# Kernel optimization log

Measured on AMD Instinct MI355X. Metric: run time of the kernel, lower is better.

The kernel has to match this reference:

```python
import jax, jax.numpy as jnp
import numpy as np

D, NH, NKV, HD, FFN = 2560, 8, 4, 256, 10240
QD = NH * HD
CTX = 4096
EPS = 1e-6


def _rms(x, eps=EPS):
    # Equivalent to F.layer_norm(cat([x,-x]), 2D): zero mean, var = mean(x^2)
    return x * jax.lax.rsqrt(jnp.mean(jnp.square(x), axis=-1, keepdims=True) + eps)


def rmsnorm(x, w):
    # Gemma-style ANERMSNorm with learnable scale (1 + w)
    return _rms(x) * (1.0 + w)


def rotate_half(x):
    x1, x2 = jnp.split(x, 2, axis=-1)
    return jnp.concatenate([-x2, x1], axis=-1)


def setup_inputs() -> dict:
    key = jax.random.key(0)
    ks = jax.random.split(key, 16)
    s = 0.02
    return {
        "x": jax.random.normal(ks[0], (1, 1, D), jnp.float32),
        "cos": jax.random.uniform(ks[1], (1, 1, HD), jnp.float32, -1.0, 1.0),
        "sin": jax.random.uniform(ks[2], (1, 1, HD), jnp.float32, -1.0, 1.0),
        "mask": jnp.zeros((1, 1, 1, CTX), jnp.float32),
        "cache_k": jax.random.normal(ks[3], (1, NKV, CTX, HD), jnp.float32),
        "cache_v": jax.random.normal(ks[4], (1, NKV, CTX, HD), jnp.float32),
        "ctx_len": CTX,
        "w_in_ln": jax.random.normal(ks[5], (D,), jnp.float32) * s,
        "w_post_attn_ln": jax.random.normal(ks[6], (D,), jnp.float32) * s,
        "w_pre_ffn_ln": jax.random.normal(ks[7], (D,), jnp.float32) * s,
        "w_post_ffn_ln": jax.random.normal(ks[8], (D,), jnp.float32) * s,
        "Wq": jax.random.normal(ks[9], (QD, D), jnp.float32) * s,
        "Wo": jax.random.normal(ks[10], (D, QD), jnp.float32) * s,
        "Wg": jax.random.normal(ks[11], (FFN, D), jnp.float32) * s,
        "Wu": jax.random.normal(ks[12], (FFN, D), jnp.float32) * s,
        "Wd": jax.random.normal(ks[13], (D, FFN), jnp.float32) * s,
    }


def reference(x, cos, sin, mask, cache_k, cache_v, ctx_len,
              w_in_ln, w_post_attn_ln, w_pre_ffn_ln, w_post_ffn_ln,
              Wq, Wo, Wg, Wu, Wd):
    rep = NH // NKV
    residual = x
    h = rmsnorm(x, w_in_ln)                      # (1,1,D)
    q = h @ Wq.T                                 # (1,1,QD)  1x1-conv == linear
    q = q.reshape(1, 1, NH, HD)
    q = _rms(q)                                  # q_norm, no learnable weight
    q = q.transpose(0, 2, 1, 3)                  # (1,NH,1,HD)
    q = q * cos[:, None] + rotate_half(q) * sin[:, None]
    k = jnp.repeat(cache_k, rep, axis=1)         # (1,NH,L,HD) GQA expand
    v = jnp.repeat(cache_v, rep, axis=1)
    scores = jnp.einsum("bhqd,bhkd->bhqk", q, k) * 1.0 + mask
    attn = jax.nn.softmax(scores, axis=-1)       # numerically stable softmax
    a = jnp.einsum("bhqk,bhkd->bhqd", attn, v)   # (1,NH,1,HD)
    a = a.transpose(0, 2, 1, 3).reshape(1, 1, QD)
    a = a @ Wo.T                                 # (1,1,D)
    x = residual + rmsnorm(a, w_post_attn_ln)
    residual = x
    h = rmsnorm(x, w_pre_ffn_ln)
    g = jax.nn.gelu(h @ Wg.T, approximate=True)  # tanh-approx GELU
    ffn = (g * (h @ Wu.T)) @ Wd.T                # GeGLU down-proj
    x = residual + rmsnorm(ffn, w_post_ffn_ln)
    return x
```

## Files before the change

kernel.cpp:

```cpp
#include <hip/hip_runtime.h>

#define D_    2560
#define NH_   8
#define NKV_  4
#define HD_   256
#define FFN_  10240
#define QD_   2048
#define CTX_  4096
#define EPSF  1e-6f
#define ACH   64

typedef float f4 __attribute__((ext_vector_type(4)));

__device__ __forceinline__ float wave_red_sum(float v) {
#pragma unroll
    for (int o = 32; o > 0; o >>= 1) v += __shfl_down(v, o, 64);
    return v;
}

__device__ __forceinline__ float wave_red_sum_b(float v) {
#pragma unroll
    for (int o = 32; o > 0; o >>= 1) v += __shfl_xor(v, o, 64);
    return v;
}

__device__ __forceinline__ float block_red_sum(float v) {
    __shared__ float s[4];
    __shared__ float tot;
    int lane = threadIdx.x & 63, w = threadIdx.x >> 6;
    v = wave_red_sum(v);
    if (lane == 0) s[w] = v;
    __syncthreads();
    if (threadIdx.x == 0) tot = s[0] + s[1] + s[2] + s[3];
    __syncthreads();
    return tot;
}

__device__ __forceinline__ float block_red_max(float v) {
    __shared__ float s[4];
    __shared__ float tot;
    int lane = threadIdx.x & 63, w = threadIdx.x >> 6;
#pragma unroll
    for (int o = 32; o > 0; o >>= 1) v = fmaxf(v, __shfl_down(v, o, 64));
    if (lane == 0) s[w] = v;
    __syncthreads();
    if (threadIdx.x == 0) tot = fmaxf(fmaxf(s[0], s[1]), fmaxf(s[2], s[3]));
    __syncthreads();
    return tot;
}

template <int CPL>
__global__ __launch_bounds__(256) void k_gemv_row(const float* __restrict__ W,
                                                  const float* __restrict__ x,
                                                  float* __restrict__ y) {
    int lane = threadIdx.x & 63;
    int row = (blockIdx.x * 256 + threadIdx.x) >> 6;
    const f4* Wr = (const f4*)W + (size_t)row * (CPL * 64) + lane;
    const f4* X = (const f4*)x + lane;
    f4 wv[CPL];
#pragma unroll
    for (int k = 0; k < CPL; k++) wv[k] = __builtin_nontemporal_load(Wr + k * 64);
    float acc = 0.f;
#pragma unroll
    for (int k = 0; k < CPL; k++) {
        f4 xx = X[k * 64];
        acc += wv[k].x * xx.x + wv[k].y * xx.y + wv[k].z * xx.z + wv[k].w * xx.w;
    }
    acc = wave_red_sum(acc);
    if (lane == 0) y[row] = acc;
}

__global__ __launch_bounds__(256) void k_geglu(const float* __restrict__ Wg,
                                               const float* __restrict__ Wu,
                                               const float* __restrict__ h,
                                               float* __restrict__ gu) {
    int lane = threadIdx.x & 63;
    int row = (blockIdx.x * 256 + threadIdx.x) >> 6;
    const f4* G = (const f4*)Wg + (size_t)row * 640 + lane;
    const f4* U = (const f4*)Wu + (size_t)row * 640 + lane;
    const f4* X = (const f4*)h + lane;
    f4 wg[10], wu[10];
#pragma unroll
    for (int k = 0; k < 10; k++) wg[k] = __builtin_nontemporal_load(G + k * 64);
#pragma unroll
    for (int k = 0; k < 10; k++) wu[k] = __builtin_nontemporal_load(U + k * 64);
    float ag = 0.f, au = 0.f;
#pragma unroll
    for (int k = 0; k < 10; k++) {
        f4 xx = X[k * 64];
        ag += wg[k].x * xx.x + wg[k].y * xx.y + wg[k].z * xx.z + wg[k].w * xx.w;
        au += wu[k].x * xx.x + wu[k].y * xx.y + wu[k].z * xx.z + wu[k].w * xx.w;
    }
#pragma unroll
    for (int o = 32; o > 0; o >>= 1) {
        ag += __shfl_down(ag, o, 64);
        au += __shfl_down(au, o, 64);
    }
    if (lane == 0) {
        float g = ag;
        float tt = tanhf(0.7978845608028654f * (g + 0.044715f * g * g * g));
        gu[row] = 0.5f * g * (1.f + tt) * au;
    }
}

__global__ __launch_bounds__(256) void k_wd(const float* __restrict__ Wd,
                                            const float* __restrict__ gu,
                                            float* __restrict__ part) {
    int lane = threadIdx.x & 63;
    int t = (blockIdx.x * 256 + threadIdx.x) >> 6;
    int half = t & 1;
    const f4* Wr = (const f4*)Wd + (size_t)t * 1280 + lane;
    const f4* X = (const f4*)gu + half * 1280 + lane;
    f4 wv[20];
#pragma unroll
    for (int k = 0; k < 20; k++) wv[k] = __builtin_nontemporal_load(Wr + k * 64);
    float acc = 0.f;
#pragma unroll
    for (int k = 0; k < 20; k++) {
        f4 xx = X[k * 64];
        acc += wv[k].x * xx.x + wv[k].y * xx.y + wv[k].z * xx.z + wv[k].w * xx.w;
    }
    acc = wave_red_sum(acc);
    if (lane == 0) part[t] = acc;
}

__global__ void k_res_rms(const float* __restrict__ res,
                          const float* __restrict__ apart, int slots,
                          const float* __restrict__ w1, float* __restrict__ out1,
                          const float* __restrict__ w2, float* __restrict__ out2) {
    const int K = D_ / 256;
    int t = threadIdx.x;
    float va[K];
    float ss = 0.f;
#pragma unroll
    for (int k = 0; k < K; k++) {
        int i = t + k * 256;
        float v = 0.f;
        for (int s = 0; s < slots; s++) v += apart[(size_t)i * slots + s];
        va[k] = v;
        ss += v * v;
    }
    float tot = block_red_sum(ss);
    float rs = rsqrtf(tot / (float)D_ + EPSF);
    float vo[K];
    float ss2 = 0.f;
#pragma unroll
    for (int k = 0; k < K; k++) {
        int i = t + k * 256;
        float r = res ? res[i] : 0.f;
        vo[k] = r + va[k] * rs * (1.f + w1[i]);
        out1[i] = vo[k];
        ss2 += vo[k] * vo[k];
    }
    if (out2) {
        float tot2 = block_red_sum(ss2);
        float rs2 = rsqrtf(tot2 / (float)D_ + EPSF);
#pragma unroll
        for (int k = 0; k < K; k++) {
            int i = t + k * 256;
            out2[i] = vo[k] * rs2 * (1.f + w2[i]);
        }
    }
}

__global__ __launch_bounds__(256) void k_attn_part(const float* __restrict__ Kc,
                                                   const float* __restrict__ V,
                                                   const float* __restrict__ qraw,
                                                   const float* __restrict__ cosv,
                                                   const float* __restrict__ sinv,
                                                   const float* __restrict__ mask,
                                                   float* __restrict__ pm,
                                                   float* __restrict__ pl,
                                                   float* __restrict__ pacc) {
    int kvh = blockIdx.x, ch = blockIdx.y;
    int lane = threadIdx.x & 63, w = threadIdx.x >> 6;
    int t = threadIdx.x;
    int h0 = 2 * kvh, h1 = h0 + 1;
    int l0 = ch * 64;
    __shared__ float s0[64], s1[64];

    const f4* q4 = (const f4*)qraw;
    f4 qr0 = q4[h0 * 64 + lane];
    f4 qr1 = q4[h1 * 64 + lane];
    float n0 = wave_red_sum_b(qr0.x * qr0.x + qr0.y * qr0.y + qr0.z * qr0.z + qr0.w * qr0.w);
    float n1 = wave_red_sum_b(qr1.x * qr1.x + qr1.y * qr1.y + qr1.z * qr1.z + qr1.w * qr1.w);
    f4 qn0 = qr0 * rsqrtf(n0 / (float)HD_ + EPSF);
    f4 qn1 = qr1 * rsqrtf(n1 / (float)HD_ + EPSF);
    f4 p0, p1;
    p0.x = __shfl_xor(qn0.x, 32, 64); p0.y = __shfl_xor(qn0.y, 32, 64);
    p0.z = __shfl_xor(qn0.z, 32, 64); p0.w = __shfl_xor(qn0.w, 32, 64);
    p1.x = __shfl_xor(qn1.x, 32, 64); p1.y = __shfl_xor(qn1.y, 32, 64);
    p1.z = __shfl_xor(qn1.z, 32, 64); p1.w = __shfl_xor(qn1.w, 32, 64);
    f4 rot0 = (lane < 32) ? -p0 : p0;
    f4 rot1 = (lane < 32) ? -p1 : p1;
    f4 cs = ((const f4*)cosv)[lane];
    f4 sn = ((const f4*)sinv)[lane];
    f4 q0 = qn0 * cs + rot0 * sn;
    f4 q1 = qn1 * cs + rot1 * sn;

    const f4* Kb = (const f4*)Kc + ((size_t)kvh * CTX_ + l0 + w * 16) * 64 + lane;
    f4 kk[16];
#pragma unroll
    for (int i = 0; i < 16; i++) kk[i] = Kb[i * 64];
    float d0[16], d1[16];
#pragma unroll
    for (int i = 0; i < 16; i++) {
        d0[i] = kk[i].x * q0.x + kk[i].y * q0.y + kk[i].z * q0.z + kk[i].w * q0.w;
        d1[i] = kk[i].x * q1.x + kk[i].y * q1.y + kk[i].z * q1.z + kk[i].w * q1.w;
    }
#pragma unroll
    for (int o = 32; o > 0; o >>= 1) {
#pragma unroll
        for (int i = 0; i < 16; i++) {
            d0[i] += __shfl_down(d0[i], o, 64);
            d1[i] += __shfl_down(d1[i], o, 64);
        }
    }
    if (lane == 0) {
#pragma unroll
        for (int i = 0; i < 16; i++) {
            float m = mask[l0 + w * 16 + i];
            s0[w * 16 + i] = d0[i] + m;
            s1[w * 16 + i] = d1[i] + m;
        }
    }
    __syncthreads();

    float m0 = block_red_max(t < 64 ? s0[t] : -3e38f);
    float m1 = block_red_max(t < 64 ? s1[t] : -3e38f);
    float e0 = 0.f, e1 = 0.f;
    if (t < 64) {
        e0 = expf(s0[t] - m0); s0[t] = e0;
        e1 = expf(s1[t] - m1); s1[t] = e1;
    }
    float l0sum = block_red_sum(e0);
    float l1sum = block_red_sum(e1);

    const float* Vb = V + ((size_t)kvh * CTX_ + l0) * HD_ + t;
    float a0 = 0.f, a1 = 0.f;
#pragma unroll 8
    for (int li = 0; li < 64; li++) {
        float v = Vb[(size_t)li * HD_];
        a0 += s0[li] * v;
        a1 += s1[li] * v;
    }
    pacc[((size_t)(h0 * ACH) + ch) * HD_ + t] = a0;
    pacc[((size_t)(h1 * ACH) + ch) * HD_ + t] = a1;
    if (t == 0) {
        pm[h0 * ACH + ch] = m0; pl[h0 * ACH + ch] = l0sum;
        pm[h1 * ACH + ch] = m1; pl[h1 * ACH + ch] = l1sum;
    }
}

__global__ __launch_bounds__(256) void k_attn_comb(const float* __restrict__ pm,
                                                   const float* __restrict__ pl,
                                                   const float* __restrict__ pacc,
                                                   float* __restrict__ a) {
    int h = blockIdx.x, t = threadIdx.x;
    __shared__ float wgt[ACH];
    float M = block_red_max(t < ACH ? pm[h * ACH + t] : -3e38f);
    float lw = 0.f;
    if (t < ACH) {
        float wv = expf(pm[h * ACH + t] - M);
        wgt[t] = wv;
        lw = wv * pl[h * ACH + t];
    }
    float L = block_red_sum(lw);
    float acc = 0.f;
    const float* pb = pacc + (size_t)h * ACH * HD_ + t;
#pragma unroll 8
    for (int c = 0; c < ACH; c++) acc += wgt[c] * pb[(size_t)c * HD_];
    a[h * HD_ + t] = acc / L;
}

extern "C" void kernel_launch(void* const* d_in, const int* in_sizes, int n_in,
                              void* d_out, int out_size, void* d_ws, size_t ws_size,
                              hipStream_t stream) {
    const float* x     = (const float*)d_in[0];
    const float* cosv  = (const float*)d_in[1];
    const float* sinv  = (const float*)d_in[2];
    const float* mask  = (const float*)d_in[3];
    const float* cK    = (const float*)d_in[4];
    const float* cV    = (const float*)d_in[5];
    const float* w_in  = (const float*)d_in[7];
    const float* w_pa  = (const float*)d_in[8];
    const float* w_pf  = (const float*)d_in[9];
    const float* w_pff = (const float*)d_in[10];
    const float* Wq    = (const float*)d_in[11];
    const float* Wo    = (const float*)d_in[12];
    const float* Wg    = (const float*)d_in[13];
    const float* Wu    = (const float*)d_in[14];
    const float* Wd    = (const float*)d_in[15];

    float* ws    = (float*)d_ws;
    float* h     = ws;
    float* qraw  = ws + 2560;
    float* pm    = ws + 4608;
    float* pl    = ws + 5120;
    float* pacc  = ws + 5632;
    float* a     = ws + 136704;
    float* ao    = ws + 138752;
    float* x2    = ws + 141312;
    float* h2    = ws + 143872;
    float* gu    = ws + 146432;
    float* partd = ws + 156672;
    float* out   = (float*)d_out;

    k_res_rms<<<1, 256, 0, stream>>>(nullptr, x, 1, w_in, h, nullptr, nullptr);
    k_gemv_row<10><<<QD_ / 4, 256, 0, stream>>>(Wq, h, qraw);
    k_attn_part<<<dim3(NKV_, ACH), 256, 0, stream>>>(cK, cV, qraw, cosv, sinv,
                                                     mask, pm, pl, pacc);
    k_attn_comb<<<NH_, 256, 0, stream>>>(pm, pl, pacc, a);
    k_gemv_row<8><<<D_ / 4, 256, 0, stream>>>(Wo, a, ao);
    k_res_rms<<<1, 256, 0, stream>>>(x, ao, 1, w_pa, x2, w_pf, h2);
    k_geglu<<<FFN_ / 4, 256, 0, stream>>>(Wg, Wu, h2, gu);
    k_wd<<<D_ * 2 / 4, 256, 0, stream>>>(Wd, gu, partd);
    k_res_rms<<<1, 256, 0, stream>>>(x2, partd, 2, w_pff, out, nullptr, nullptr);
}
```

Measured before the change: 99.58 us.

## Fuse input RMSNorm into Wq GEMV and vectorize attention V accumulation

Removes the standalone single-block input RMSNorm launch by having each Wq GEMV wave recompute the norm of x redundantly before the dot product. In the attention partial kernel, each wave now loads 16 V rows as float4 and accumulates them, then the waves' partial sums are reduced through shared memory. This replaces the per-thread scalar loop over 64 rows. The remaining residual-RMSNorm kernels use 512 threads to shorten the serial single-block work. The trade-off is redundant norm computation per wave plus extra shared memory and a sync in the attention kernel.

```diff
diff --git a/kernel.cpp b/kernel.cpp
--- a/kernel.cpp
+++ b/kernel.cpp
@@ -24,29 +24,73 @@
     return v;
 }
 
+template <int NW>
 __device__ __forceinline__ float block_red_sum(float v) {
-    __shared__ float s[4];
+    __shared__ float s[NW];
     __shared__ float tot;
     int lane = threadIdx.x & 63, w = threadIdx.x >> 6;
     v = wave_red_sum(v);
     if (lane == 0) s[w] = v;
     __syncthreads();
-    if (threadIdx.x == 0) tot = s[0] + s[1] + s[2] + s[3];
+    if (threadIdx.x == 0) {
+        float t = 0.f;
+#pragma unroll
+        for (int i = 0; i < NW; i++) t += s[i];
+        tot = t;
+    }
     __syncthreads();
     return tot;
 }
 
+template <int NW>
 __device__ __forceinline__ float block_red_max(float v) {
-    __shared__ float s[4];
+    __shared__ float s[NW];
     __shared__ float tot;
     int lane = threadIdx.x & 63, w = threadIdx.x >> 6;
 #pragma unroll
     for (int o = 32; o > 0; o >>= 1) v = fmaxf(v, __shfl_down(v, o, 64));
     if (lane == 0) s[w] = v;
     __syncthreads();
-    if (threadIdx.x == 0) tot = fmaxf(fmaxf(s[0], s[1]), fmaxf(s[2], s[3]));
+    if (threadIdx.x == 0) {
+        float t = -3e38f;
+#pragma unroll
+        for (int i = 0; i < NW; i++) t = fmaxf(t, s[i]);
+        tot = t;
+    }
     __syncthreads();
     return tot;
+}
+
+__global__ __launch_bounds__(256) void k_wq_fused(const float* __restrict__ Wq,
+                                                  const float* __restrict__ x,
+                                                  const float* __restrict__ w_in,
+                                                  float* __restrict__ qraw) {
+    int lane = threadIdx.x & 63;
+    int row = (blockIdx.x * 256 + threadIdx.x) >> 6;
+    const f4* Wr = (const f4*)Wq + (size_t)row * 640 + lane;
+    const f4* X = (const f4*)x + lane;
+    const f4* WI = (const f4*)w_in + lane;
+    f4 wv[10];
+#pragma unroll
+    for (int k = 0; k < 10; k++) wv[k] = __builtin_nontemporal_load(Wr + k * 64);
+    f4 xx[10];
+#pragma unroll
+    for (int k = 0; k < 10; k++) xx[k] = X[k * 64];
+    float ss = 0.f;
+#pragma unroll
+    for (int k = 0; k < 10; k++)
+        ss += xx[k].x * xx[k].x + xx[k].y * xx[k].y + xx[k].z * xx[k].z + xx[k].w * xx[k].w;
+    ss = wave_red_sum_b(ss);
+    float rs = rsqrtf(ss / (float)D_ + EPSF);
+    float acc = 0.f;
+#pragma unroll
+    for (int k = 0; k < 10; k++) {
+        f4 wi = WI[k * 64];
+        f4 hh = xx[k] * rs * (1.f + wi);
+        acc += wv[k].x * hh.x + wv[k].y * hh.y + wv[k].z * hh.z + wv[k].w * hh.w;
+    }
+    acc = wave_red_sum(acc);
+    if (lane == 0) qraw[row] = acc;
 }
 
 template <int CPL>
@@ -124,40 +168,40 @@
     if (lane == 0) part[t] = acc;
 }
 
-__global__ void k_res_rms(const float* __restrict__ res,
-                          const float* __restrict__ apart, int slots,
-                          const float* __restrict__ w1, float* __restrict__ out1,
-                          const float* __restrict__ w2, float* __restrict__ out2) {
-    const int K = D_ / 256;
+__global__ __launch_bounds__(512) void k_res_rms(const float* __restrict__ res,
+                                                 const float* __restrict__ apart, int slots,
+                                                 const float* __restrict__ w1, float* __restrict__ out1,
+                                                 const float* __restrict__ w2, float* __restrict__ out2) {
+    const int K = D_ / 512;
     int t = threadIdx.x;
     float va[K];
     float ss = 0.f;
 #pragma unroll
     for (int k = 0; k < K; k++) {
-        int i = t + k * 256;
+        int i = t + k * 512;
         float v = 0.f;
         for (int s = 0; s < slots; s++) v += apart[(size_t)i * slots + s];
         va[k] = v;
         ss += v * v;
     }
-    float tot = block_red_sum(ss);
+    float tot = block_red_sum<8>(ss);
     float rs = rsqrtf(tot / (float)D_ + EPSF);
     float vo[K];
     float ss2 = 0.f;
 #pragma unroll
     for (int k = 0; k < K; k++) {
-        int i = t + k * 256;
+        int i = t + k * 512;
         float r = res ? res[i] : 0.f;
         vo[k] = r + va[k] * rs * (1.f + w1[i]);
         out1[i] = vo[k];
         ss2 += vo[k] * vo[k];
     }
     if (out2) {
-        float tot2 = block_red_sum(ss2);
+        float tot2 = block_red_sum<8>(ss2);
         float rs2 = rsqrtf(tot2 / (float)D_ + EPSF);
 #pragma unroll
         for (int k = 0; k < K; k++) {
-            int i = t + k * 256;
+            int i = t + k * 512;
             out2[i] = vo[k] * rs2 * (1.f + w2[i]);
         }
     }
@@ -178,6 +222,7 @@
     int h0 = 2 * kvh, h1 = h0 + 1;
     int l0 = ch * 64;
     __shared__ float s0[64], s1[64];
+    __shared__ f4 pv0[4][64], pv1[4][64];
 
     const f4* q4 = (const f4*)qraw;
     f4 qr0 = q4[h0 * 64 + lane];
@@ -226,26 +271,35 @@
     }
     __syncthreads();
 
-    float m0 = block_red_max(t < 64 ? s0[t] : -3e38f);
-    float m1 = block_red_max(t < 64 ? s1[t] : -3e38f);
+    float m0 = block_red_max<4>(t < 64 ? s0[t] : -3e38f);
+    float m1 = block_red_max<4>(t < 64 ? s1[t] : -3e38f);
     float e0 = 0.f, e1 = 0.f;
     if (t < 64) {
         e0 = expf(s0[t] - m0); s0[t] = e0;
         e1 = expf(s1[t] - m1); s1[t] = e1;
     }
-    float l0sum = block_red_sum(e0);
-    float l1sum = block_red_sum(e1);
-
-    const float* Vb = V + ((size_t)kvh * CTX_ + l0) * HD_ + t;
-    float a0 = 0.f, a1 = 0.f;
-#pragma unroll 8
-    for (int li = 0; li < 64; li++) {
-        float v = Vb[(size_t)li * HD_];
-        a0 += s0[li] * v;
-        a1 += s1[li] * v;
-    }
-    pacc[((size_t)(h0 * ACH) + ch) * HD_ + t] = a0;
-    pacc[((size_t)(h1 * ACH) + ch) * HD_ + t] = a1;
+    float l0sum = block_red_sum<4>(e0);
+    float l1sum = block_red_sum<4>(e1);
+
+    const f4* Vb = (const f4*)V + ((size_t)kvh * CTX_ + l0 + w * 16) * 64 + lane;
+    f4 vv[16];
+#pragma unroll
+    for (int i = 0; i < 16; i++) vv[i] = Vb[i * 64];
+    f4 a0 = {0.f, 0.f, 0.f, 0.f}, a1 = {0.f, 0.f, 0.f, 0.f};
+#pragma unroll
+    for (int i = 0; i < 16; i++) {
+        a0 += vv[i] * s0[w * 16 + i];
+        a1 += vv[i] * s1[w * 16 + i];
+    }
+    pv0[w][lane] = a0;
+    pv1[w][lane] = a1;
+    __syncthreads();
+    const float* f0 = (const float*)pv0;
+    const float* f1 = (const float*)pv1;
+    float r0 = f0[t] + f0[256 + t] + f0[512 + t] + f0[768 + t];
+    float r1 = f1[t] + f1[256 + t] + f1[512 + t] + f1[768 + t];
+    pacc[((size_t)(h0 * ACH) + ch) * HD_ + t] = r0;
+    pacc[((size_t)(h1 * ACH) + ch) * HD_ + t] = r1;
     if (t == 0) {
         pm[h0 * ACH + ch] = m0; pl[h0 * ACH + ch] = l0sum;
         pm[h1 * ACH + ch] = m1; pl[h1 * ACH + ch] = l1sum;
@@ -258,14 +312,14 @@
                                                    float* __restrict__ a) {
     int h = blockIdx.x, t = threadIdx.x;
     __shared__ float wgt[ACH];
-    float M = block_red_max(t < ACH ? pm[h * ACH + t] : -3e38f);
+    float M = block_red_max<4>(t < ACH ? pm[h * ACH + t] : -3e38f);
     float lw = 0.f;
     if (t < ACH) {
         float wv = expf(pm[h * ACH + t] - M);
         wgt[t] = wv;
         lw = wv * pl[h * ACH + t];
     }
-    float L = block_red_sum(lw);
+    float L = block_red_sum<4>(lw);
     float acc = 0.f;
     const float* pb = pacc + (size_t)h * ACH * HD_ + t;
 #pragma unroll 8
@@ -293,27 +347,25 @@
     const float* Wd    = (const float*)d_in[15];
 
     float* ws    = (float*)d_ws;
-    float* h     = ws;
-    float* qraw  = ws + 2560;
-    float* pm    = ws + 4608;
-    float* pl    = ws + 5120;
-    float* pacc  = ws + 5632;
-    float* a     = ws + 136704;
-    float* ao    = ws + 138752;
-    float* x2    = ws + 141312;
-    float* h2    = ws + 143872;
-    float* gu    = ws + 146432;
-    float* partd = ws + 156672;
+    float* qraw  = ws;
+    float* pm    = ws + 2048;
+    float* pl    = ws + 2560;
+    float* pacc  = ws + 3072;
+    float* a     = ws + 134144;
+    float* ao    = ws + 136192;
+    float* x2    = ws + 138752;
+    float* h2    = ws + 141312;
+    float* gu    = ws + 143872;
+    float* partd = ws + 154112;
     float* out   = (float*)d_out;
 
-    k_res_rms<<<1, 256, 0, stream>>>(nullptr, x, 1, w_in, h, nullptr, nullptr);
-    k_gemv_row<10><<<QD_ / 4, 256, 0, stream>>>(Wq, h, qraw);
+    k_wq_fused<<<QD_ / 4, 256, 0, stream>>>(Wq, x, w_in, qraw);
     k_attn_part<<<dim3(NKV_, ACH), 256, 0, stream>>>(cK, cV, qraw, cosv, sinv,
                                                      mask, pm, pl, pacc);
     k_attn_comb<<<NH_, 256, 0, stream>>>(pm, pl, pacc, a);
     k_gemv_row<8><<<D_ / 4, 256, 0, stream>>>(Wo, a, ao);
-    k_res_rms<<<1, 256, 0, stream>>>(x, ao, 1, w_pa, x2, w_pf, h2);
+    k_res_rms<<<1, 512, 0, stream>>>(x, ao, 1, w_pa, x2, w_pf, h2);
     k_geglu<<<FFN_ / 4, 256, 0, stream>>>(Wg, Wu, h2, gu);
     k_wd<<<D_ * 2 / 4, 256, 0, stream>>>(Wd, gu, partd);
-    k_res_rms<<<1, 256, 0, stream>>>(x2, partd, 2, w_pff, out, nullptr, nullptr);
-}
+    k_res_rms<<<1, 512, 0, stream>>>(x2, partd, 2, w_pff, out, nullptr, nullptr);
+}
```

Measured after the change: 91.35 us. 8.3% less time.
